# Kernel optimization log

Measured on AMD Instinct MI355X. Metric: run time of the kernel, lower is better.

Reference implementation:

```python
import jax, jax.numpy as jnp
import numpy as np

K = 11  # masked conv3d kernel size

def mask_A(k):
    # mask type 'A': flattened (i,j,t) positions with current_id < k^3//2 + 1
    # (current_id starts at 1) -> first k^3//2 positions are 1.
    m = (np.arange(k ** 3) < (k ** 3) // 2).astype(np.float32).reshape(k, k, k)
    return jnp.asarray(m)

def conv3d(x, w, b, pad):
    out = jax.lax.conv_general_dilated(
        x, w, window_strides=(1, 1, 1), padding=[(pad, pad)] * 3,
        dimension_numbers=('NCDHW', 'OIDHW', 'NCDHW'))
    return out + b[None, :, None, None, None]

def conv2d(x, w, b, pad):
    out = jax.lax.conv_general_dilated(
        x, w, window_strides=(1, 1), padding=[(pad, pad)] * 2,
        dimension_numbers=('NCHW', 'OIHW', 'NCHW'))
    return out + b[None, :, None, None]

def pconv(x, w, b):
    # 1x1x1 conv3d as channel GEMM; w: [O, C]
    return jnp.einsum('bcdhw,oc->bodhw', x, w) + b[None, :, None, None, None]

def _phi(z):
    return 0.5 * (1.0 + jax.lax.erf(z / jnp.sqrt(2.0).astype(z.dtype)))

def setup_inputs() -> dict:
    key = jax.random.key(0)
    ks = jax.random.split(key, 12)
    M = 192
    B, H, W = 1, 48, 48
    s = 0.02
    x = jax.random.normal(ks[0], (B, M, H, W), jnp.float32)
    hyper = jax.random.normal(ks[1], (B, 2 * M, H, W), jnp.float32)
    W3 = s * jax.random.normal(ks[2], (M, 2 * M, 3, 3), jnp.float32)
    b3 = jnp.zeros((M,), jnp.float32)
    W1 = s * jax.random.normal(ks[3], (24, 1, K, K, K), jnp.float32)
    b1 = jnp.zeros((24,), jnp.float32)
    Wa = s * jax.random.normal(ks[4], (48, 25), jnp.float32)
    ba = jnp.zeros((48,), jnp.float32)
    Wb = s * jax.random.normal(ks[5], (96, 48), jnp.float32)
    bb = jnp.zeros((96,), jnp.float32)
    Wc = s * jax.random.normal(ks[6], (9, 96), jnp.float32)
    bc = jnp.zeros((9,), jnp.float32)
    return {"x": x, "hyper": hyper, "W3": W3, "b3": b3, "W1": W1, "b1": b1,
            "Wa": Wa, "ba": ba, "Wb": Wb, "bb": bb, "Wc": Wc, "bc": bc}

def reference(x, hyper, W3, b3, W1, b1, Wa, ba, Wb, bb, Wc, bc):
    # x: [B,M,H,W], hyper: [B,2M,H,W]
    x5 = x[:, None]                                   # [B,1,M,H,W]
    h = conv2d(hyper, W3, b3, 1)[:, None]             # [B,1,M,H,W]
    W1m = W1 * mask_A(K)[None, None]                  # causal mask re-applied each fwd
    x1 = conv3d(x5, W1m, b1, 5)                       # [B,24,M,H,W]
    t = jnp.concatenate([x1, h], axis=1)              # [B,25,M,H,W]
    t = jax.nn.relu(pconv(t, Wa, ba))                 # [B,48,M,H,W]
    t = jax.nn.relu(pconv(t, Wb, bb))                 # [B,96,M,H,W]
    out = pconv(t, Wc, bc)                            # [B,9,M,H,W]
    # 3-component weighted Gaussian entropy model
    mu = out[:, 0:3]
    sc = out[:, 3:6]
    sc = jnp.abs(jnp.where(sc == 0.0, 1e-9, sc))
    w = jax.nn.softmax(out[:, 6:9], axis=1)
    xe = x[:, None]                                   # [B,1,M,H,W]
    lik = jnp.abs(_phi((xe + 0.5 - mu) / sc) - _phi((xe - 0.5 - mu) / sc))
    p3 = jnp.sum(w * lik, axis=1)                     # [B,M,H,W]
    return (p3, out)
```

## Files before the change

### kernel.cpp

```cpp
#include <hip/hip_runtime.h>
#include <hip/hip_fp16.h>
#include <math.h>

#define HW    2304
#define NPOS  442368

typedef _Float16 f16x8 __attribute__((ext_vector_type(8)));
typedef __fp16   h16x2 __attribute__((ext_vector_type(2)));
typedef float    f32x4 __attribute__((ext_vector_type(4)));

__device__ __forceinline__ float phi_f(float z) {
    return 0.5f * (1.0f + erff(z * 0.70710678118654752f));
}
__device__ __forceinline__ unsigned short f2h(float v) {
    _Float16 h = (_Float16)v;
    return *reinterpret_cast<unsigned short*>(&h);
}
__device__ __forceinline__ unsigned int pk2(float a, float b) {
    return (unsigned int)f2h(a) | ((unsigned int)f2h(b) << 16);
}
__device__ __forceinline__ unsigned int pkrtz(float a, float b) {
    h16x2 h = __builtin_amdgcn_cvt_pkrtz(a, b);
    return *reinterpret_cast<unsigned int*>(&h);
}

__global__ __launch_bounds__(256) void prep_all(const float* __restrict__ hyper,
                                                const float* __restrict__ W3,
                                                const float* __restrict__ W1,
                                                const float* __restrict__ Wa,
                                                const float* __restrict__ ba,
                                                const float* __restrict__ b1,
                                                const float* __restrict__ Wb,
                                                const float* __restrict__ bb,
                                                const float* __restrict__ Wc,
                                                const float* __restrict__ xg,
                                                unsigned short* __restrict__ hyperTp,
                                                unsigned short* __restrict__ apack,
                                                unsigned short* __restrict__ pk,
                                                unsigned short* __restrict__ xhp) {
    const int bx = blockIdx.x;
    if (bx < 948) {
        __shared__ float s[32][33];
        const int pt = bx % 79, it = bx / 79;
        const int tid = threadIdx.x;
        const int c = tid & 31, r = tid >> 5;
        const int pp = pt * 32 + c;
        const int yp = pp / 50, xp = pp % 50;
        const bool inter = (pp < 2500) && yp >= 1 && yp <= 48 && xp >= 1 && xp <= 48;
        const int src = inter ? ((yp - 1) * 48 + (xp - 1)) : 0;
#pragma unroll
        for (int i = 0; i < 4; ++i) {
            int icl = r + i * 8;
            s[icl][c] = inter ? hyper[(size_t)(it * 32 + icl) * HW + src] : 0.f;
        }
        __syncthreads();
#pragma unroll
        for (int i = 0; i < 4; ++i) {
            int pl = r + i * 8;
            int pp2 = pt * 32 + pl;
            if (pp2 < 2500)
                hyperTp[(size_t)pp2 * 384 + it * 32 + c] = f2h(s[c][pl]);
        }
    } else if (bx < 3540) {
        int idx = (bx - 948) * 256 + threadIdx.x;
        int j = idx & 7;
        int l = (idx >> 3) & 63;
        int rest = idx >> 9;
        int t = rest % 9; rest /= 9;
        int c = rest % 12; int T = rest / 12;
        int oc = T * 16 + (l & 15);
        int ic = c * 32 + (l >> 4) * 8 + j;
        apack[idx] = f2h(W3[((size_t)oc * 384 + ic) * 9 + t]);
    } else if (bx < 3700) {
        int idx = (bx - 3540) * 256 + threadIdx.x;
        if (idx >= 40960) return;
        float v = 0.f;
        if (idx < 31744) {
            int j = idx & 7, lane = (idx >> 3) & 63, s = (idx >> 9) & 1, c = idx >> 10;
            int q = lane >> 4;
            int oc = s * 16 + (lane & 15);
            int r = 2 * c + (q >> 1), h = q & 1, kw = 8 * h + j;
            if (oc < 24 && r < 61 && kw < 11) {
                int kd = r / 11, kh = r % 11;
                int tap = kd * 121 + kh * 11 + kw;
                if (tap < 665) v = W1[oc * 1331 + tap];
            }
        } else if (idx < 33280) {
            int i2 = idx - 31744;
            int j = i2 & 7, lane = (i2 >> 3) & 63, t = i2 >> 9;
            int m = t * 16 + (lane & 15), k = (lane >> 4) * 8 + j;
            if (k < 25) v = Wa[m * 25 + k];
            else if (k == 25) {
                float s = ba[m];
                for (int c = 0; c < 24; ++c) s += Wa[m * 25 + c] * b1[c];
                v = s;
            }
        } else if (idx < 39424) {
            int i3 = idx - 33280;
            int j = i3 & 7, lane = (i3 >> 3) & 63, k2 = (i3 >> 9) & 1, s = i3 >> 10;
            int m = s * 16 + (lane & 15), ch = k2 * 32 + (lane >> 4) * 8 + j;
            if (ch < 48) v = Wb[m * 48 + ch];
            else if (ch == 48) v = bb[m];
        } else {
            int i4 = idx - 39424;
            int j = i4 & 7, lane = (i4 >> 3) & 63, k3 = i4 >> 9;
            int m = lane & 15, ch = k3 * 32 + (lane >> 4) * 8 + j;
            if (m < 9) v = Wc[m * 96 + ch];
        }
        pk[idx] = f2h(v);
    } else {
        int idx = (bx - 3700) * 256 + threadIdx.x;
        if (idx >= 187456) return;
        int si = idx * 4;
        int zp = si / 3712, rem = si - zp * 3712;
        int yp = rem >> 6, xp0 = rem & 63;
        float f[4];
#pragma unroll
        for (int k = 0; k < 4; ++k) {
            int xp = xp0 + k;
            bool in = zp >= 5 && zp < 197 && yp >= 5 && yp < 53 && xp >= 5 && xp < 53;
            f[k] = in ? xg[(size_t)(zp - 5) * HW + (yp - 5) * 48 + (xp - 5)] : 0.f;
        }
        *(uint2*)&xhp[si] = make_uint2(pk2(f[0], f[1]), pk2(f[2], f[3]));
    }
}

__global__ __launch_bounds__(256) void conv2d_mfma(const unsigned short* __restrict__ hyperTp,
                                                   const unsigned short* __restrict__ apack,
                                                   const float* __restrict__ b3,
                                                   float* __restrict__ hbuf) {
    const int T = blockIdx.x;
    const int tid = threadIdx.x, w = tid >> 6, lane = tid & 63;
    const int n = lane & 15, q = lane >> 4;
    const int g = blockIdx.y * 4 + w;
    const int yy = g / 3, xb = (g % 3) * 16;
    const size_t base = (size_t)(yy * 50 + xb + n) * 384 + q * 8;

    f32x4 acc = {};
    for (int c = 0; c < 12; ++c) {
        const unsigned short* ap = apack + ((size_t)(T * 12 + c) * 9) * 512 + lane * 8;
        const int coff = c * 32;
#pragma unroll
        for (int t = 0; t < 9; ++t) {
            f16x8 a = *(const f16x8*)(ap + t * 512);
            const int dd = (t / 3) * 50 + (t % 3);
            f16x8 b = *(const f16x8*)(hyperTp + base + (size_t)dd * 384 + coff);
            acc = __builtin_amdgcn_mfma_f32_16x16x32_f16(a, b, acc, 0, 0, 0);
        }
    }
#pragma unroll
    for (int e = 0; e < 4; ++e) {
        int oc = T * 16 + q * 4 + e;
        hbuf[(size_t)oc * HW + yy * 48 + xb + n] = acc[e] + b3[oc];
    }
}

#define PSTR 40
__global__ __launch_bounds__(256) void conv3d_mlp(const unsigned short* __restrict__ xhp,
                                                  const unsigned short* __restrict__ pk,
                                                  const float* __restrict__ hbuf,
                                                  const float* __restrict__ xg,
                                                  const float* __restrict__ bc,
                                                  float* __restrict__ out) {
    __shared__ __align__(16) unsigned char smem[31792];
    unsigned short* P = (unsigned short*)smem;
    unsigned short* S = (unsigned short*)smem;
    const int tid = threadIdx.x, w = tid >> 6, lane = tid & 63;
    const int n = lane & 15, q = lane >> 4;
    const int x0 = blockIdx.x * 16, y0 = blockIdx.y, d0 = blockIdx.z * 16;
    unsigned short* tw = (unsigned short*)(smem + 18480) + w * 1664;
    unsigned short* t1s = tw;
    unsigned short* t2s = tw;
    float*          oacs = (float*)tw;

#pragma unroll
    for (int k = 0; k < 4; ++k) {
        int idx = tid + k * 256;
        if (idx < 924) {
            int row = idx >> 2, quarter = idx & 3;
            int py = row / 21, pz = row - py * 21;
            const uint4* src = (const uint4*)(xhp + ((size_t)(d0 + pz) * 58 + (y0 + py)) * 64
                                              + x0 + quarter * 8);
            *(uint4*)&P[row * PSTR + quarter * 8] = *src;
        }
    }
    __syncthreads();

    const f32x4 zf = {0.f, 0.f, 0.f, 0.f};
    f32x4 acc[4][2];
#pragma unroll
    for (int p = 0; p < 4; ++p) { acc[p][0] = zf; acc[p][1] = zf; }

    const f16x8* Av = (const f16x8*)pk;
    f16x8 a0 = Av[lane], a1 = Av[64 + lane];
    for (int c = 0; c < 31; ++c) {
        f16x8 ca0 = a0, ca1 = a1;
        int cn = (c < 30) ? c + 1 : 30;
        a0 = Av[cn * 128 + lane];
        a1 = Av[cn * 128 + 64 + lane];
        int r = 2 * c + (q >> 1);
        int kd = r / 11, kh = r - kd * 11;
        const unsigned short* rowp = P + (kh * 21 + (n + kd)) * PSTR + 4 * w + (q & 1) * 8;
        unsigned int u[6];
        *(uint2*)&u[0] = *(const uint2*)(rowp);
        *(uint2*)&u[2] = *(const uint2*)(rowp + 4);
        *(uint2*)&u[4] = *(const uint2*)(rowp + 8);
#pragma unroll
        for (int px = 0; px < 4; ++px) {
            unsigned int bw[4];
#pragma unroll
            for (int i = 0; i < 4; ++i) {
                if ((px & 1) == 0) bw[i] = u[(px >> 1) + i];
                else bw[i] = (u[(px >> 1) + i] >> 16) | (u[(px >> 1) + 1 + i] << 16);
            }
            f16x8 bf = *(f16x8*)bw;
            acc[px][0] = __builtin_amdgcn_mfma_f32_16x16x32_f16(ca0, bf, acc[px][0], 0, 0, 0);
            acc[px][1] = __builtin_amdgcn_mfma_f32_16x16x32_f16(ca1, bf, acc[px][1], 0, 0, 0);
        }
    }
    __syncthreads();

#pragma unroll
    for (int px = 0; px < 4; ++px) {
        unsigned int lo = pk2(acc[px][0][0], acc[px][0][1]);
        unsigned int hi = pk2(acc[px][0][2], acc[px][0][3]);
        *(uint2*)&S[(w * 16 + n) * 136 + px * 32 + q * 4] = make_uint2(lo, hi);
        if (q < 2) {
            unsigned int l2 = pk2(acc[px][1][0], acc[px][1][1]);
            unsigned int h2 = pk2(acc[px][1][2], acc[px][1][3]);
            *(uint2*)&S[(w * 16 + n) * 136 + px * 32 + 16 + q * 4] = make_uint2(l2, h2);
        }
    }
    {
        const int pxl = lane >> 4, dep = lane & 15;
        float hv = hbuf[(size_t)(d0 + dep) * HW + y0 * 48 + x0 + 4 * w + pxl];
        *(uint4*)&S[(w * 16 + dep) * 136 + pxl * 32 + 24] =
            make_uint4(pk2(hv, 1.0f), 0u, 0u, 0u);
    }

    const f16x8* WaF = (const f16x8*)(pk + 31744);
    const f16x8* WbF = (const f16x8*)(pk + 33280);
    const f16x8* WcF = (const f16x8*)(pk + 39424);
    f16x8 waf[3], wbf[12], wcf[3];
#pragma unroll
    for (int s = 0; s < 3; ++s) waf[s] = WaF[s * 64 + lane];
#pragma unroll
    for (int t = 0; t < 12; ++t) wbf[t] = WbF[t * 64 + lane];
#pragma unroll
    for (int k = 0; k < 3; ++k) wcf[k] = WcF[k * 64 + lane];
    float bcv[4];
#pragma unroll
    for (int e = 0; e < 4; ++e) bcv[e] = (q * 4 + e < 9) ? bc[q * 4 + e] : 0.f;

#pragma unroll
    for (int px = 0; px < 4; ++px) {
        f16x8 b0 = *(const f16x8*)&S[(w * 16 + n) * 136 + px * 32 + q * 8];
        {
            unsigned int lo = (q == 0) ? 0x00003C00u : 0u;
            *(uint2*)&t1s[n * 72 + 48 + q * 4] = make_uint2(lo, 0u);
        }
#pragma unroll
        for (int s = 0; s < 3; ++s) {
            f32x4 r1 = __builtin_amdgcn_mfma_f32_16x16x32_f16(waf[s], b0, zf, 0, 0, 0);
            *(uint2*)&t1s[n * 72 + s * 16 + q * 4] =
                make_uint2(pkrtz(fmaxf(r1[0], 0.f), fmaxf(r1[1], 0.f)),
                           pkrtz(fmaxf(r1[2], 0.f), fmaxf(r1[3], 0.f)));
        }
        f32x4 rb[6];
#pragma unroll
        for (int s = 0; s < 6; ++s) rb[s] = zf;
#pragma unroll
        for (int k2 = 0; k2 < 2; ++k2) {
            f16x8 bf = *(const f16x8*)&t1s[n * 72 + k2 * 32 + q * 8];
#pragma unroll
            for (int s = 0; s < 6; ++s)
                rb[s] = __builtin_amdgcn_mfma_f32_16x16x32_f16(wbf[s * 2 + k2], bf, rb[s], 0, 0, 0);
        }
#pragma unroll
        for (int s = 0; s < 6; ++s)
            *(uint2*)&t2s[n * 104 + s * 16 + q * 4] =
                make_uint2(pkrtz(fmaxf(rb[s][0], 0.f), fmaxf(rb[s][1], 0.f)),
                           pkrtz(fmaxf(rb[s][2], 0.f), fmaxf(rb[s][3], 0.f)));
        f32x4 rc = zf;
#pragma unroll
        for (int k3 = 0; k3 < 3; ++k3) {
            f16x8 bf = *(const f16x8*)&t2s[n * 104 + k3 * 32 + q * 8];
            rc = __builtin_amdgcn_mfma_f32_16x16x32_f16(wcf[k3], bf, rc, 0, 0, 0);
        }
#pragma unroll
        for (int e = 0; e < 4; ++e) {
            int row = q * 4 + e;
            if (row < 9) oacs[n * 13 + row] = rc[e] + bcv[e];
        }
        if (lane < 16) {
            float o[9];
#pragma unroll
            for (int jj = 0; jj < 9; ++jj) o[jj] = oacs[lane * 13 + jj];
            const size_t gp = (size_t)(d0 + lane) * HW + y0 * 48 + x0 + 4 * w + px;
            float xv = xg[gp];
            float m = fmaxf(o[6], fmaxf(o[7], o[8]));
            float e0 = expf(o[6] - m), e1 = expf(o[7] - m), e2 = expf(o[8] - m);
            float inv_es = 1.0f / (e0 + e1 + e2);
            float p = 0.f;
#pragma unroll
            for (int jj = 0; jj < 3; ++jj) {
                float mu = o[jj];
                float sc = o[3 + jj];
                sc = (sc == 0.0f) ? 1e-9f : sc;
                sc = fabsf(sc);
                float a = phi_f((xv + 0.5f - mu) / sc);
                float b = phi_f((xv - 0.5f - mu) / sc);
                float lik = fabsf(a - b);
                float wgt = ((jj == 0) ? e0 : (jj == 1) ? e1 : e2) * inv_es;
                p = fmaf(wgt, lik, p);
            }
            out[gp] = p;
#pragma unroll
            for (int jj = 0; jj < 9; ++jj) out[NPOS + (size_t)jj * NPOS + gp] = o[jj];
        }
    }
}

extern "C" void kernel_launch(void* const* d_in, const int* in_sizes, int n_in,
                              void* d_out, int out_size, void* d_ws, size_t ws_size,
                              hipStream_t stream) {
    const float* x     = (const float*)d_in[0];
    const float* hyper = (const float*)d_in[1];
    const float* W3    = (const float*)d_in[2];
    const float* b3    = (const float*)d_in[3];
    const float* W1    = (const float*)d_in[4];
    const float* b1    = (const float*)d_in[5];
    const float* Wa    = (const float*)d_in[6];
    const float* ba    = (const float*)d_in[7];
    const float* Wb    = (const float*)d_in[8];
    const float* bb    = (const float*)d_in[9];
    const float* Wc    = (const float*)d_in[10];
    const float* bc    = (const float*)d_in[11];
    float* out = (float*)d_out;

    float* hbuf = (float*)d_ws;
    unsigned short* hyperTp = (unsigned short*)(hbuf + NPOS);
    unsigned short* apack   = hyperTp + 960000;
    unsigned short* pk      = apack + 663552;
    unsigned short* xhp     = pk + 40960;

    prep_all<<<4433, 256, 0, stream>>>(hyper, W3, W1, Wa, ba, b1, Wb, bb, Wc, x,
                                       hyperTp, apack, pk, xhp);
    conv2d_mfma<<<dim3(12, 36), 256, 0, stream>>>(hyperTp, apack, b3, hbuf);
    conv3d_mlp<<<dim3(3, 48, 12), 256, 0, stream>>>(xhp, pk, hbuf, x, bc, out);
}
```

Before: 180.6 us.

## Fuse hyper conv2d into conv3d_mlp kernel with split-K across waves

New measurement: 177.3 us. Within noise of the previous version (-1.8%).

```diff
diff --git a/kernel.cpp b/kernel.cpp
--- a/kernel.cpp
+++ b/kernel.cpp
@@ -125,40 +125,12 @@
     }
 }
 
-__global__ __launch_bounds__(256) void conv2d_mfma(const unsigned short* __restrict__ hyperTp,
-                                                   const unsigned short* __restrict__ apack,
-                                                   const float* __restrict__ b3,
-                                                   float* __restrict__ hbuf) {
-    const int T = blockIdx.x;
-    const int tid = threadIdx.x, w = tid >> 6, lane = tid & 63;
-    const int n = lane & 15, q = lane >> 4;
-    const int g = blockIdx.y * 4 + w;
-    const int yy = g / 3, xb = (g % 3) * 16;
-    const size_t base = (size_t)(yy * 50 + xb + n) * 384 + q * 8;
-
-    f32x4 acc = {};
-    for (int c = 0; c < 12; ++c) {
-        const unsigned short* ap = apack + ((size_t)(T * 12 + c) * 9) * 512 + lane * 8;
-        const int coff = c * 32;
-#pragma unroll
-        for (int t = 0; t < 9; ++t) {
-            f16x8 a = *(const f16x8*)(ap + t * 512);
-            const int dd = (t / 3) * 50 + (t % 3);
-            f16x8 b = *(const f16x8*)(hyperTp + base + (size_t)dd * 384 + coff);
-            acc = __builtin_amdgcn_mfma_f32_16x16x32_f16(a, b, acc, 0, 0, 0);
-        }
-    }
-#pragma unroll
-    for (int e = 0; e < 4; ++e) {
-        int oc = T * 16 + q * 4 + e;
-        hbuf[(size_t)oc * HW + yy * 48 + xb + n] = acc[e] + b3[oc];
-    }
-}
-
 #define PSTR 40
 __global__ __launch_bounds__(256) void conv3d_mlp(const unsigned short* __restrict__ xhp,
                                                   const unsigned short* __restrict__ pk,
-                                                  const float* __restrict__ hbuf,
+                                                  const unsigned short* __restrict__ hyperTp,
+                                                  const unsigned short* __restrict__ apack,
+                                                  const float* __restrict__ b3,
                                                   const float* __restrict__ xg,
                                                   const float* __restrict__ bc,
                                                   float* __restrict__ out) {
@@ -168,6 +140,8 @@
     const int tid = threadIdx.x, w = tid >> 6, lane = tid & 63;
     const int n = lane & 15, q = lane >> 4;
     const int x0 = blockIdx.x * 16, y0 = blockIdx.y, d0 = blockIdx.z * 16;
+    const int T = blockIdx.z;
+    float* part = (float*)(smem + 18480);
     unsigned short* tw = (unsigned short*)(smem + 18480) + w * 1664;
     unsigned short* t1s = tw;
     unsigned short* t2s = tw;
@@ -218,6 +192,19 @@
             acc[px][1] = __builtin_amdgcn_mfma_f32_16x16x32_f16(ca1, bf, acc[px][1], 0, 0, 0);
         }
     }
+
+    {
+        const size_t base2 = (size_t)(y0 * 50 + x0 + n) * 384 + q * 8;
+        f32x4 hacc = zf;
+        for (int kk = 27 * w; kk < 27 * w + 27; ++kk) {
+            int c2 = kk / 9, t2 = kk - c2 * 9;
+            f16x8 a = *(const f16x8*)(apack + (((size_t)T * 12 + c2) * 9 + t2) * 512 + lane * 8);
+            int dd = (t2 / 3) * 50 + (t2 % 3);
+            f16x8 b = *(const f16x8*)(hyperTp + base2 + (size_t)dd * 384 + c2 * 32);
+            hacc = __builtin_amdgcn_mfma_f32_16x16x32_f16(a, b, hacc, 0, 0, 0);
+        }
+        *(f32x4*)&part[(w * 64 + lane) * 4] = hacc;
+    }
     __syncthreads();
 
 #pragma unroll
@@ -232,11 +219,16 @@
         }
     }
     {
-        const int pxl = lane >> 4, dep = lane & 15;
-        float hv = hbuf[(size_t)(d0 + dep) * HW + y0 * 48 + x0 + 4 * w + pxl];
-        *(uint4*)&S[(w * 16 + dep) * 136 + pxl * 32 + 24] =
+        const int pl = lane >> 4, dep = lane & 15;
+        const int p = 4 * w + pl;
+        const int lane_p = p + 16 * (dep >> 2), e = dep & 3;
+        float hv = part[(0 * 64 + lane_p) * 4 + e] + part[(1 * 64 + lane_p) * 4 + e]
+                 + part[(2 * 64 + lane_p) * 4 + e] + part[(3 * 64 + lane_p) * 4 + e];
+        hv += b3[T * 16 + dep];
+        *(uint4*)&S[(w * 16 + dep) * 136 + pl * 32 + 24] =
             make_uint4(pk2(hv, 1.0f), 0u, 0u, 0u);
     }
+    __syncthreads();
 
     const f16x8* WaF = (const f16x8*)(pk + 31744);
     const f16x8* WbF = (const f16x8*)(pk + 33280);
@@ -338,14 +330,13 @@
     const float* bc    = (const float*)d_in[11];
     float* out = (float*)d_out;
 
-    float* hbuf = (float*)d_ws;
-    unsigned short* hyperTp = (unsigned short*)(hbuf + NPOS);
+    unsigned short* hyperTp = (unsigned short*)d_ws;
     unsigned short* apack   = hyperTp + 960000;
     unsigned short* pk      = apack + 663552;
     unsigned short* xhp     = pk + 40960;
 
     prep_all<<<4433, 256, 0, stream>>>(hyper, W3, W1, Wa, ba, b1, Wb, bb, Wc, x,
                                        hyperTp, apack, pk, xhp);
-    conv2d_mfma<<<dim3(12, 36), 256, 0, stream>>>(hyperTp, apack, b3, hbuf);
-    conv3d_mlp<<<dim3(3, 48, 12), 256, 0, stream>>>(xhp, pk, hbuf, x, bc, out);
-}
+    conv3d_mlp<<<dim3(3, 48, 12), 256, 0, stream>>>(xhp, pk, hyperTp, apack, b3,
+                                                    x, bc, out);
+}
```
